# Optimization experiments

Measured on AMD Instinct MI355X. Metric: run time of the kernel, lower is better.

Reference implementation:

```python
import jax, jax.numpy as jnp
import numpy as np
import math

H = 1024
E = 8
K = 2
CF = 1.5
THR = 0.5


def setup_inputs() -> dict:
    key = jax.random.key(0)
    ks = jax.random.split(key, 8)
    s = 0.02
    return {
        'hidden_states': jax.random.normal(ks[0], (2, 2048, H), jnp.float32),
        # importance predictor: Linear(H, H//2) -> ReLU -> Linear(H//2, 1) -> Sigmoid
        'wi1': jax.random.normal(ks[1], (H, H // 2), jnp.float32) * s,
        'bi1': jnp.zeros((H // 2,), jnp.float32),
        'wi2': jax.random.normal(ks[2], (H // 2, 1), jnp.float32) * s,
        'bi2': jnp.zeros((1,), jnp.float32),
        # router_important: Linear(H,H) -> ReLU -> Linear(H,E)
        'wr1': jax.random.normal(ks[3], (H, H), jnp.float32) * s,
        'br1': jnp.zeros((H,), jnp.float32),
        'wr2': jax.random.normal(ks[4], (H, E), jnp.float32) * s,
        'br2': jnp.zeros((E,), jnp.float32),
        # router_unimportant: Linear(H,H) -> ReLU -> Linear(H,E)
        'wu1': jax.random.normal(ks[5], (H, H), jnp.float32) * s,
        'bu1': jnp.zeros((H,), jnp.float32),
        'wu2': jax.random.normal(ks[6], (H, E), jnp.float32) * s,
        'bu2': jnp.zeros((E,), jnp.float32),
    }


def reference(hidden_states, wi1, bi1, wi2, bi2, wr1, br1, wr2, br2, wu1, bu1, wu2, bu2):
    x = hidden_states
    B, S, _ = x.shape
    N = B * S
    capacity = int(B * S * CF * K / E)  # static per-expert capacity

    # dual-gate routing
    importance = jax.nn.sigmoid(jnp.maximum(x @ wi1 + bi1, 0.0) @ wi2 + bi2)  # [B,S,1]
    imp_mask = (importance > THR).astype(x.dtype)                              # [B,S,1]
    logits_imp = jnp.maximum(x @ wr1 + br1, 0.0) @ wr2 + br2                   # [B,S,E]
    logits_unimp = jnp.maximum(x @ wu1 + bu1, 0.0) @ wu2 + bu2                 # [B,S,E]
    router_logits = imp_mask * logits_imp + (1.0 - imp_mask) * logits_unimp
    router_probs = jax.nn.softmax(router_logits, axis=-1)                      # [B,S,E]

    top_k_probs, top_k_indices = jax.lax.top_k(router_probs, K)
    top_k_probs = top_k_probs / top_k_probs.sum(-1, keepdims=True)

    # capacity-constrained dispatch: k-major assignment order (outer loop over k,
    # tokens in order), position within expert = running count, drop if >= capacity
    ef = top_k_indices.reshape(N, K).T.reshape(-1)   # [K*N] expert id, k-major
    pf = top_k_probs.reshape(N, K).T.reshape(-1)     # [K*N] gate prob
    tf = jnp.tile(jnp.arange(N), K)                  # [K*N] token id
    oh = jax.nn.one_hot(ef, E, dtype=jnp.int32)      # [K*N, E]
    pos = jnp.take_along_axis(jnp.cumsum(oh, axis=0), ef[:, None], 1)[:, 0] - 1
    keep = pos < capacity
    posc = jnp.clip(pos, 0, capacity - 1)

    zeros = jnp.zeros((N, E, capacity), x.dtype)
    dispatch = zeros.at[tf, ef, posc].add(keep.astype(x.dtype))
    combine = zeros.at[tf, ef, posc].add(jnp.where(keep, pf, 0.0))
    dispatch = dispatch.reshape(B, S, E, capacity)
    combine = combine.reshape(B, S, E, capacity)

    # aux losses
    rppe = router_probs.mean((0, 1))
    entropy_loss = jnp.sum(rppe * jnp.log(rppe * E + 1e-9))
    imp_sum = (router_probs * imp_mask).sum((0, 1)) + 1e-9
    ippe = imp_sum / imp_sum.sum()
    imp_entropy = -jnp.sum(ippe * jnp.log(ippe + 1e-9))
    aux_loss = entropy_loss - 0.1 * (imp_entropy / math.log(E))

    return dispatch, combine, router_probs, aux_loss, importance
```

## Files before the change

kernel.cpp:

```cpp
#include <hip/hip_runtime.h>
#include <math.h>

#define HDIM  1024
#define HHALF 512
#define NEXP  8
#define NTOK  4096
#define CAP   1536
#define NTOT  2560
#define TOTAL_DC (2u * NTOK * NEXP * CAP)

typedef _Float16 f16x8 __attribute__((ext_vector_type(8)));
typedef float    f32x4 __attribute__((ext_vector_type(4)));

#define GEMM_BLOCKS 640
#define FILL_BLOCKS 1408
#define S_LO 2048.0f
#define S_W  32.0f

__global__ __launch_bounds__(256) void prep(
    const float* __restrict__ x,
    const float* __restrict__ wi1, const float* __restrict__ wr1,
    const float* __restrict__ wu1,
    const float* __restrict__ bi1, const float* __restrict__ br1,
    const float* __restrict__ bu1,
    _Float16* __restrict__ Ah, _Float16* __restrict__ Al,
    _Float16* __restrict__ Bth, _Float16* __restrict__ Btl,
    float* __restrict__ bias_cat)
{
    __shared__ float tile[64][65];
    const int bid = blockIdx.x, tid = threadIdx.x;

    if (bid < 2048) {
        const int i8 = bid * 256 + tid;
        const float4* x4 = (const float4*)x;
        float4 v0 = x4[i8 * 2];
        float4 v1 = x4[i8 * 2 + 1];
        float f[8] = {v0.x, v0.y, v0.z, v0.w, v1.x, v1.y, v1.z, v1.w};
        f16x8 hi, lo;
#pragma unroll
        for (int j = 0; j < 8; j++) {
            _Float16 h = (_Float16)f[j];
            hi[j] = h;
            lo[j] = (_Float16)((f[j] - (float)h) * S_LO);
        }
        *(f16x8*)&Ah[(size_t)i8 * 8] = hi;
        *(f16x8*)&Al[(size_t)i8 * 8] = lo;
        return;
    }
    if (bid < 2688) {
        int local; const float* src; int C, nof;
        int b = bid - 2048;
        if (b < 128)      { src = wi1; C = 512;  nof = 0;    local = b; }
        else if (b < 384) { src = wr1; C = 1024; nof = 512;  local = b - 128; }
        else              { src = wu1; C = 1024; nof = 1536; local = b - 384; }
        const int nti = local >> 4, kti = local & 15;
#pragma unroll
        for (int p = 0; p < 16; p++) {
            int e = p * 256 + tid;
            int kr = e >> 6, nc = e & 63;
            tile[kr][nc] = src[(size_t)(kti * 64 + kr) * C + nti * 64 + nc];
        }
        __syncthreads();
#pragma unroll
        for (int p = 0; p < 16; p++) {
            int e = p * 256 + tid;
            int nl = e >> 6, kk = e & 63;
            float w32 = tile[kk][nl] * S_W;
            _Float16 h = (_Float16)w32;
            _Float16 l = (_Float16)((w32 - (float)h) * S_LO);
            const size_t o = (size_t)(nof + nti * 64 + nl) * 1024 + kti * 64 + kk;
            Bth[o] = h;
            Btl[o] = l;
        }
        return;
    }
    for (int i = tid; i < NTOT; i += 256) {
        float v = (i < 512) ? bi1[i] : (i < 1536) ? br1[i - 512] : bu1[i - 1536];
        bias_cat[i] = v;
    }
}

__global__ __launch_bounds__(256, 2) void gemm_fill(
    const _Float16* __restrict__ Ah, const _Float16* __restrict__ Al,
    const _Float16* __restrict__ Bth, const _Float16* __restrict__ Btl,
    const float* __restrict__ bias_cat,
    const float* __restrict__ wi2, const float* __restrict__ wr2,
    const float* __restrict__ wu2,
    float* __restrict__ part, float* __restrict__ out)
{
    if (blockIdx.x >= GEMM_BLOCKS) {
        f32x4* o4 = (f32x4*)out;
        const unsigned total4 = TOTAL_DC / 4;
        unsigned i = (blockIdx.x - GEMM_BLOCKS) * 256u + threadIdx.x;
        const unsigned stride = FILL_BLOCKS * 256u;
        const f32x4 z = {0.f, 0.f, 0.f, 0.f};
        for (; i < total4; i += stride)
            __builtin_nontemporal_store(z, o4 + i);
        return;
    }

    __shared__ _Float16 lds[2][4][128][32];

    const int tid = threadIdx.x;
    const int lane = tid & 63, wid = tid >> 6;

    const int xcd = blockIdx.x & 7;
    const int idx = blockIdx.x >> 3;
    const int bm  = xcd * 4 + (idx & 3);
    const int bn  = idx >> 2;
    const int rowBase = bm * 128, colBase = bn * 128;

    const _Float16* gb =
        (wid == 0) ? Ah  + (size_t)rowBase * 1024 :
        (wid == 1) ? Al  + (size_t)rowBase * 1024 :
        (wid == 2) ? Bth + (size_t)colBase * 1024 :
                     Btl + (size_t)colBase * 1024;
    const int lrow = lane >> 2;
    const int lkg  = lane & 3;

    f32x4 acc_hh[4][4], acc_x[4][4];
    const f32x4 z4 = {0.f, 0.f, 0.f, 0.f};
#pragma unroll
    for (int i = 0; i < 4; i++)
#pragma unroll
        for (int j = 0; j < 4; j++) { acc_hh[i][j] = z4; acc_x[i][j] = z4; }

    const int mw = (wid >> 1) * 64, nw = (wid & 1) * 64;
    const int fr = lane & 15, s = lane >> 4;

#define STAGE(buf, k0)                                                        \
    {                                                                         \
        _Pragma("unroll")                                                     \
        for (int i = 0; i < 8; i++) {                                         \
            const int r = i * 16 + lrow;                                      \
            __builtin_amdgcn_global_load_lds(                                 \
                (const void*)(gb + (size_t)r * 1024 + (k0) + lkg * 8),        \
                (void*)&lds[buf][wid][i * 16][0], 16, 0, 0);                  \
        }                                                                     \
    }

#define COMPUTE(buf)                                                          \
    {                                                                         \
        f16x8 fa_h[4], fa_l[4], fb_h[4], fb_l[4];                             \
        _Pragma("unroll")                                                     \
        for (int mf = 0; mf < 4; mf++) {                                      \
            fa_h[mf] = *(const f16x8*)&lds[buf][0][mw + mf * 16 + fr][s * 8]; \
            fa_l[mf] = *(const f16x8*)&lds[buf][1][mw + mf * 16 + fr][s * 8]; \
        }                                                                     \
        _Pragma("unroll")                                                     \
        for (int nf = 0; nf < 4; nf++) {                                      \
            fb_h[nf] = *(const f16x8*)&lds[buf][2][nw + nf * 16 + fr][s * 8]; \
            fb_l[nf] = *(const f16x8*)&lds[buf][3][nw + nf * 16 + fr][s * 8]; \
        }                                                                     \
        _Pragma("unroll")                                                     \
        for (int mf = 0; mf < 4; mf++)                                        \
            _Pragma("unroll")                                                 \
            for (int nf = 0; nf < 4; nf++) {                                  \
                acc_hh[mf][nf] = __builtin_amdgcn_mfma_f32_16x16x32_f16(      \
                    fa_h[mf], fb_h[nf], acc_hh[mf][nf], 0, 0, 0);             \
                acc_x[mf][nf] = __builtin_amdgcn_mfma_f32_16x16x32_f16(       \
                    fa_h[mf], fb_l[nf], acc_x[mf][nf], 0, 0, 0);              \
                acc_x[mf][nf] = __builtin_amdgcn_mfma_f32_16x16x32_f16(       \
                    fa_l[mf], fb_h[nf], acc_x[mf][nf], 0, 0, 0);              \
            }                                                                 \
    }

    STAGE(0, 0);
    __syncthreads();

    for (int t = 0; t < 32; t += 2) {
        if (t + 1 < 32) STAGE(1, (t + 1) * 32);
        COMPUTE(0);
        __syncthreads();
        if (t + 2 < 32) STAGE(0, (t + 2) * 32);
        COMPUTE(1);
        __syncthreads();
    }
#undef STAGE
#undef COMPUTE

    const int seg = (bn < 4) ? 0 : (bn < 12 ? 1 : 2);
    const int half = wid & 1;
    float w2v[4][8];
    float bcol[4];
#pragma unroll
    for (int nf = 0; nf < 4; nf++) {
        const int c = colBase + nw + nf * 16 + fr;
        bcol[nf] = bias_cat[c];
        if (seg == 0) {
            w2v[nf][0] = wi2[c];
        } else if (seg == 1) {
            const float4* w4 = (const float4*)&wr2[(c - 512) * 8];
            float4 a = w4[0], b = w4[1];
            w2v[nf][0] = a.x; w2v[nf][1] = a.y; w2v[nf][2] = a.z; w2v[nf][3] = a.w;
            w2v[nf][4] = b.x; w2v[nf][5] = b.y; w2v[nf][6] = b.z; w2v[nf][7] = b.w;
        } else {
            const float4* w4 = (const float4*)&wu2[(c - 1536) * 8];
            float4 a = w4[0], b = w4[1];
            w2v[nf][0] = a.x; w2v[nf][1] = a.y; w2v[nf][2] = a.z; w2v[nf][3] = a.w;
            w2v[nf][4] = b.x; w2v[nf][5] = b.y; w2v[nf][6] = b.z; w2v[nf][7] = b.w;
        }
    }

    const int tgroup = lane >> 4;
#pragma unroll
    for (int mf = 0; mf < 4; mf++) {
        const int tok0 = rowBase + mw + mf * 16 + tgroup * 4;
#pragma unroll
        for (int r = 0; r < 4; r++) {
            float sacc[8];
#pragma unroll
            for (int e = 0; e < 8; e++) sacc[e] = 0.f;
#pragma unroll
            for (int nf = 0; nf < 4; nf++) {
                float v = (acc_hh[mf][nf][r] + acc_x[mf][nf][r] * (1.0f / S_LO))
                          * (1.0f / S_W) + bcol[nf];
                v = fmaxf(v, 0.f);
                if (seg == 0) {
                    sacc[0] = fmaf(v, w2v[nf][0], sacc[0]);
                } else {
#pragma unroll
                    for (int e = 0; e < 8; e++)
                        sacc[e] = fmaf(v, w2v[nf][e], sacc[e]);
                }
            }
            const int nE = (seg == 0) ? 1 : 8;
            for (int e = 0; e < nE; e++) {
                float xv = sacc[e];
                xv += __shfl_xor(xv, 1, 64);
                xv += __shfl_xor(xv, 2, 64);
                xv += __shfl_xor(xv, 4, 64);
                xv += __shfl_xor(xv, 8, 64);
                if (fr == 0)
                    part[(((size_t)bn * 2 + half) * NTOK + (tok0 + r)) * 8 + e] = xv;
            }
        }
    }
}

__global__ __launch_bounds__(256) void reduce_route(
    const float* __restrict__ part,
    const float* __restrict__ bi2, const float* __restrict__ br2,
    const float* __restrict__ bu2,
    float* __restrict__ oprobs, float* __restrict__ oimp,
    int* __restrict__ tke, float* __restrict__ tkp)
{
    const int t = blockIdx.x * 256 + threadIdx.x;

    float imp = bi2[0];
#pragma unroll
    for (int sl = 0; sl < 8; sl++)
        imp += part[((size_t)sl * NTOK + t) * 8];

    float lr[8], lu[8];
#pragma unroll
    for (int e = 0; e < 8; e++) { lr[e] = br2[e]; lu[e] = bu2[e]; }
#pragma unroll
    for (int sl = 8; sl < 24; sl++) {
        const float4* p4 = (const float4*)&part[((size_t)sl * NTOK + t) * 8];
        float4 a = p4[0], b = p4[1];
        lr[0] += a.x; lr[1] += a.y; lr[2] += a.z; lr[3] += a.w;
        lr[4] += b.x; lr[5] += b.y; lr[6] += b.z; lr[7] += b.w;
    }
#pragma unroll
    for (int sl = 24; sl < 40; sl++) {
        const float4* p4 = (const float4*)&part[((size_t)sl * NTOK + t) * 8];
        float4 a = p4[0], b = p4[1];
        lu[0] += a.x; lu[1] += a.y; lu[2] += a.z; lu[3] += a.w;
        lu[4] += b.x; lu[5] += b.y; lu[6] += b.z; lu[7] += b.w;
    }

    const float sig = 1.f / (1.f + expf(-imp));
    oimp[t] = sig;
    const bool m = sig > 0.5f;
    float lg[8];
#pragma unroll
    for (int e = 0; e < 8; e++) lg[e] = m ? lr[e] : lu[e];

    float mx = lg[0];
#pragma unroll
    for (int e = 1; e < 8; e++) mx = fmaxf(mx, lg[e]);
    float p[8], sum = 0.f;
#pragma unroll
    for (int e = 0; e < 8; e++) { p[e] = expf(lg[e] - mx); sum += p[e]; }
    const float inv = 1.f / sum;
#pragma unroll
    for (int e = 0; e < 8; e++) { p[e] *= inv; oprobs[t * 8 + e] = p[e]; }

    int i1 = 0;
#pragma unroll
    for (int e = 1; e < 8; e++) if (p[e] > p[i1]) i1 = e;
    int i2 = (i1 == 0) ? 1 : 0;
#pragma unroll
    for (int e = 0; e < 8; e++) if (e != i1 && p[e] > p[i2]) i2 = e;
    const float ps = p[i1] + p[i2];
    tke[t]        = i1;
    tke[NTOK + t] = i2;
    tkp[t]        = p[i1] / ps;
    tkp[NTOK + t] = p[i2] / ps;
}

__global__ __launch_bounds__(256) void scan_scatter_aux(
    const int* __restrict__ tke, const float* __restrict__ tkp,
    const float* __restrict__ oprobs, const float* __restrict__ oimp,
    float* __restrict__ out, float* __restrict__ oaux)
{
    __shared__ unsigned char se[2 * NTOK];
    __shared__ float         sp[2 * NTOK];
    __shared__ int  cnts[256][8];
    __shared__ float red[4][16];

    const int tid = threadIdx.x;
    const int lane = tid & 63, wv = tid >> 6;

    for (int i = tid; i < 2 * NTOK; i += 256) {
        se[i] = (unsigned char)tke[i];
        sp[i] = tkp[i];
    }

    float ap[8], ai[8];
#pragma unroll
    for (int e = 0; e < 8; e++) { ap[e] = 0.f; ai[e] = 0.f; }
    for (int t = tid; t < NTOK; t += 256) {
        const float msk = (oimp[t] > 0.5f) ? 1.f : 0.f;
#pragma unroll
        for (int e = 0; e < 8; e++) {
            float p = oprobs[t * 8 + e];
            ap[e] += p;
            ai[e] = fmaf(msk, p, ai[e]);
        }
    }
#pragma unroll
    for (int off = 32; off > 0; off >>= 1) {
#pragma unroll
        for (int e = 0; e < 8; e++) {
            ap[e] += __shfl_down(ap[e], off, 64);
            ai[e] += __shfl_down(ai[e], off, 64);
        }
    }
    if (lane == 0) {
#pragma unroll
        for (int e = 0; e < 8; e++) { red[wv][e] = ap[e]; red[wv][8 + e] = ai[e]; }
    }
    __syncthreads();
    if (tid == 0) {
        float ent = 0.f, tot = 0.f, isv[8];
#pragma unroll
        for (int e = 0; e < 8; e++) {
            float spr = red[0][e] + red[1][e] + red[2][e] + red[3][e];
            float sm  = red[0][8 + e] + red[1][8 + e] + red[2][8 + e] + red[3][8 + e];
            float r = spr / (float)NTOK;
            ent += r * logf(r * 8.f + 1e-9f);
            isv[e] = sm + 1e-9f;
            tot += isv[e];
        }
        float ie = 0.f;
#pragma unroll
        for (int e = 0; e < 8; e++) {
            float q = isv[e] / tot;
            ie -= q * logf(q + 1e-9f);
        }
        oaux[0] = ent - 0.1f * (ie / logf(8.f));
    }

    const int base = tid * 32;
    int c[8];
#pragma unroll
    for (int e = 0; e < 8; e++) c[e] = 0;
    for (int i = 0; i < 32; i++) {
        int e = se[base + i];
#pragma unroll
        for (int k = 0; k < 8; k++) c[k] += (e == k) ? 1 : 0;
    }
#pragma unroll
    for (int e = 0; e < 8; e++) cnts[tid][e] = c[e];
    __syncthreads();

    if (tid < 8) {
        int run = 0;
        for (int i = 0; i < 256; i++) {
            int v = cnts[i][tid];
            cnts[i][tid] = run;
            run += v;
        }
    }
    __syncthreads();

    int basecnt[8];
#pragma unroll
    for (int e = 0; e < 8; e++) basecnt[e] = cnts[tid][e];

    float* comb = out + (size_t)NTOK * NEXP * CAP;

    for (int i = 0; i < 32; i++) {
        const int idx = base + i;
        const int e = se[idx];
        int pos = 0;
#pragma unroll
        for (int k = 0; k < 8; k++)
            if (e == k) { pos = basecnt[k]; basecnt[k]++; }
        if (pos < CAP) {
            const int tok = idx & (NTOK - 1);
            const size_t o = ((size_t)tok * NEXP + e) * CAP + pos;
            out[o]  = 1.0f;
            comb[o] = sp[idx];
        }
    }
}

__global__ __launch_bounds__(256) void gemm_bias_relu(
    const float* __restrict__ A, const float* __restrict__ B,
    const float* __restrict__ bias, float* __restrict__ Hout, int N)
{
    __shared__ float As[16][132];
    __shared__ float Bs[16][132];
    const int tid = threadIdx.x;
    const int tx = tid & 15, ty = tid >> 4;
    const int rowBase = blockIdx.y * 128, colBase = blockIdx.x * 128;
    const int lrow = tid >> 1, lkq = (tid & 1) * 8;
    const int bkk = tid >> 4, bcol = (tid & 15) * 8;
    float acc[8][8];
#pragma unroll
    for (int i = 0; i < 8; i++)
#pragma unroll
        for (int j = 0; j < 8; j++) acc[i][j] = 0.f;
    const float* Aptr = A + (size_t)(rowBase + lrow) * HDIM + lkq;
    const float* Bptr = B + (size_t)bkk * N + colBase + bcol;
    for (int k0 = 0; k0 < HDIM; k0 += 16) {
        float4 a0 = *(const float4*)(Aptr + k0);
        float4 a1 = *(const float4*)(Aptr + k0 + 4);
        float4 b0 = *(const float4*)(Bptr + (size_t)k0 * N);
        float4 b1 = *(const float4*)(Bptr + (size_t)k0 * N + 4);
        __syncthreads();
        As[lkq + 0][lrow] = a0.x; As[lkq + 1][lrow] = a0.y;
        As[lkq + 2][lrow] = a0.z; As[lkq + 3][lrow] = a0.w;
        As[lkq + 4][lrow] = a1.x; As[lkq + 5][lrow] = a1.y;
        As[lkq + 6][lrow] = a1.z; As[lkq + 7][lrow] = a1.w;
        *(float4*)&Bs[bkk][bcol] = b0;
        *(float4*)&Bs[bkk][bcol + 4] = b1;
        __syncthreads();
#pragma unroll
        for (int kk = 0; kk < 16; kk++) {
            float4 x0 = *(const float4*)&As[kk][ty * 8];
            float4 x1 = *(const float4*)&As[kk][ty * 8 + 4];
            float4 y0 = *(const float4*)&Bs[kk][tx * 8];
            float4 y1 = *(const float4*)&Bs[kk][tx * 8 + 4];
            float av[8] = {x0.x, x0.y, x0.z, x0.w, x1.x, x1.y, x1.z, x1.w};
            float bv[8] = {y0.x, y0.y, y0.z, y0.w, y1.x, y1.y, y1.z, y1.w};
#pragma unroll
            for (int i = 0; i < 8; i++)
#pragma unroll
                for (int j = 0; j < 8; j++)
                    acc[i][j] = fmaf(av[i], bv[j], acc[i][j]);
        }
    }
#pragma unroll
    for (int i = 0; i < 8; i++) {
        const int r = rowBase + ty * 8 + i, c = colBase + tx * 8;
#pragma unroll
        for (int j = 0; j < 8; j += 4) {
            float4 v;
            v.x = fmaxf(acc[i][j + 0] + bias[c + j + 0], 0.f);
            v.y = fmaxf(acc[i][j + 1] + bias[c + j + 1], 0.f);
            v.z = fmaxf(acc[i][j + 2] + bias[c + j + 2], 0.f);
            v.w = fmaxf(acc[i][j + 3] + bias[c + j + 3], 0.f);
            *(float4*)&Hout[(size_t)r * N + c + j] = v;
        }
    }
}

__global__ __launch_bounds__(256) void zerofill_fb(float* __restrict__ out)
{
    f32x4* o4 = (f32x4*)out;
    const unsigned total4 = TOTAL_DC / 4;
    unsigned i = blockIdx.x * 256u + threadIdx.x;
    const unsigned stride = gridDim.x * 256u;
    const f32x4 z = {0.f, 0.f, 0.f, 0.f};
    for (; i < total4; i += stride) o4[i] = z;
}

__global__ __launch_bounds__(256) void second_layer_sep(
    const float* __restrict__ h_i, const float* __restrict__ h_r,
    const float* __restrict__ h_u,
    const float* __restrict__ wi2, const float* __restrict__ bi2,
    const float* __restrict__ wr2, const float* __restrict__ br2,
    const float* __restrict__ wu2, const float* __restrict__ bu2,
    float* __restrict__ oprobs, float* __restrict__ oimp,
    int* __restrict__ tke, float* __restrict__ tkp)
{
    const int t = blockIdx.x;
    const int tid = threadIdx.x;
    float pi = 0.f;
    float pr[8], pu[8];
#pragma unroll
    for (int e = 0; e < 8; e++) { pr[e] = 0.f; pu[e] = 0.f; }
    const float* hi = h_i + (size_t)t * HHALF;
    const float* hr = h_r + (size_t)t * HDIM;
    const float* hu = h_u + (size_t)t * HDIM;
    for (int j = tid; j < HHALF; j += 256) pi = fmaf(hi[j], wi2[j], pi);
    for (int j = tid; j < HDIM; j += 256) {
        float a = hr[j], b = hu[j];
#pragma unroll
        for (int e = 0; e < 8; e++) {
            pr[e] = fmaf(a, wr2[j * 8 + e], pr[e]);
            pu[e] = fmaf(b, wu2[j * 8 + e], pu[e]);
        }
    }
#pragma unroll
    for (int off = 32; off > 0; off >>= 1) {
        pi += __shfl_down(pi, off, 64);
#pragma unroll
        for (int e = 0; e < 8; e++) {
            pr[e] += __shfl_down(pr[e], off, 64);
            pu[e] += __shfl_down(pu[e], off, 64);
        }
    }
    __shared__ float red[4][17];
    const int lane = tid & 63, wv = tid >> 6;
    if (lane == 0) {
        red[wv][0] = pi;
#pragma unroll
        for (int e = 0; e < 8; e++) { red[wv][1 + e] = pr[e]; red[wv][9 + e] = pu[e]; }
    }
    __syncthreads();
    if (tid == 0) {
        float si = red[0][0] + red[1][0] + red[2][0] + red[3][0] + bi2[0];
        float sig = 1.f / (1.f + expf(-si));
        oimp[t] = sig;
        const bool m = sig > 0.5f;
        float lg[8];
#pragma unroll
        for (int e = 0; e < 8; e++) {
            float vr = red[0][1 + e] + red[1][1 + e] + red[2][1 + e] + red[3][1 + e] + br2[e];
            float vu = red[0][9 + e] + red[1][9 + e] + red[2][9 + e] + red[3][9 + e] + bu2[e];
            lg[e] = m ? vr : vu;
        }
        float mx = lg[0];
#pragma unroll
        for (int e = 1; e < 8; e++) mx = fmaxf(mx, lg[e]);
        float p[8], s = 0.f;
#pragma unroll
        for (int e = 0; e < 8; e++) { p[e] = expf(lg[e] - mx); s += p[e]; }
        const float inv = 1.f / s;
#pragma unroll
        for (int e = 0; e < 8; e++) { p[e] *= inv; oprobs[t * 8 + e] = p[e]; }
        int i1 = 0;
#pragma unroll
        for (int e = 1; e < 8; e++) if (p[e] > p[i1]) i1 = e;
        int i2 = (i1 == 0) ? 1 : 0;
#pragma unroll
        for (int e = 0; e < 8; e++) if (e != i1 && p[e] > p[i2]) i2 = e;
        const float ps = p[i1] + p[i2];
        tke[t]        = i1;
        tke[NTOK + t] = i2;
        tkp[t]        = p[i1] / ps;
        tkp[NTOK + t] = p[i2] / ps;
    }
}

extern "C" void kernel_launch(void* const* d_in, const int* in_sizes, int n_in,
                              void* d_out, int out_size, void* d_ws, size_t ws_size,
                              hipStream_t stream) {
    const float* x   = (const float*)d_in[0];
    const float* wi1 = (const float*)d_in[1];
    const float* bi1 = (const float*)d_in[2];
    const float* wi2 = (const float*)d_in[3];
    const float* bi2 = (const float*)d_in[4];
    const float* wr1 = (const float*)d_in[5];
    const float* br1 = (const float*)d_in[6];
    const float* wr2 = (const float*)d_in[7];
    const float* br2 = (const float*)d_in[8];
    const float* wu1 = (const float*)d_in[9];
    const float* bu1 = (const float*)d_in[10];
    const float* wu2 = (const float*)d_in[11];
    const float* bu2 = (const float*)d_in[12];

    float* out    = (float*)d_out;
    float* oprobs = out + (size_t)TOTAL_DC;
    float* oaux   = oprobs + NTOK * NEXP;
    float* oimp   = oaux + 1;

    const size_t szA  = (size_t)NTOK * HDIM * 2;
    const size_t szB  = (size_t)NTOT * HDIM * 2;
    const size_t szP  = (size_t)40 * NTOK * 8 * 4;
    const size_t need = 2 * szA + 2 * szB + NTOT * 4 + szP
                      + 2 * NTOK * 4 + 2 * NTOK * 4 + 4096;
    dim3 blk(256);

    if (ws_size >= need) {
        char* p = (char*)d_ws;
        _Float16* Ah   = (_Float16*)p;         p += szA;
        _Float16* Al   = (_Float16*)p;         p += szA;
        _Float16* Bth  = (_Float16*)p;         p += szB;
        _Float16* Btl  = (_Float16*)p;         p += szB;
        float*    bias = (float*)p;            p += NTOT * 4;
        float*    part = (float*)p;            p += szP;
        int*      tke  = (int*)p;              p += 2 * NTOK * 4;
        float*    tkp  = (float*)p;

        prep<<<2689, blk, 0, stream>>>(x, wi1, wr1, wu1, bi1, br1, bu1,
                                       Ah, Al, Bth, Btl, bias);
        gemm_fill<<<GEMM_BLOCKS + FILL_BLOCKS, blk, 0, stream>>>(
            Ah, Al, Bth, Btl, bias, wi2, wr2, wu2, part, out);
        reduce_route<<<NTOK / 256, blk, 0, stream>>>(
            part, bi2, br2, bu2, oprobs, oimp, tke, tkp);
        scan_scatter_aux<<<1, blk, 0, stream>>>(tke, tkp, oprobs, oimp, out, oaux);
    } else {
        float* h_i = out;
        float* h_r = h_i + (size_t)NTOK * HHALF;
        float* h_u = h_r + (size_t)NTOK * HDIM;
        int*   tke  = (int*)d_ws;
        float* tkp  = (float*)d_ws + 2 * NTOK;

        gemm_bias_relu<<<dim3(HHALF / 128, NTOK / 128), blk, 0, stream>>>(x, wi1, bi1, h_i, HHALF);
        gemm_bias_relu<<<dim3(HDIM / 128, NTOK / 128), blk, 0, stream>>>(x, wr1, br1, h_r, HDIM);
        gemm_bias_relu<<<dim3(HDIM / 128, NTOK / 128), blk, 0, stream>>>(x, wu1, bu1, h_u, HDIM);
        second_layer_sep<<<NTOK, blk, 0, stream>>>(h_i, h_r, h_u, wi2, bi2, wr2, br2,
                                                   wu2, bu2, oprobs, oimp, tke, tkp);
        zerofill_fb<<<2048, blk, 0, stream>>>(out);
        scan_scatter_aux<<<1, blk, 0, stream>>>(tke, tkp, oprobs, oimp, out, oaux);
    }
}
```

Measured before the change: 186.1 us.

## Interleave GEMM and zero-fill blocks and XOR-swizzle LDS tile layout

```diff
diff --git a/kernel.cpp b/kernel.cpp
--- a/kernel.cpp
+++ b/kernel.cpp
@@ -12,7 +12,6 @@
 typedef _Float16 f16x8 __attribute__((ext_vector_type(8)));
 typedef float    f32x4 __attribute__((ext_vector_type(4)));
 
-#define GEMM_BLOCKS 640
 #define FILL_BLOCKS 1408
 #define S_LO 2048.0f
 #define S_W  32.0f
@@ -88,10 +87,17 @@
     const float* __restrict__ wu2,
     float* __restrict__ part, float* __restrict__ out)
 {
-    if (blockIdx.x >= GEMM_BLOCKS) {
+    const int o = blockIdx.x >> 3, sub = blockIdx.x & 7;
+    const int k = o >> 3, j = o & 7;
+    int g = -1, fo = 0;
+    if (k < 11)       { if (j < 7) g = k * 7 + j; else fo = k; }
+    else if (k == 11) { if (j < 3) g = 77 + j;    else fo = 11 + (j - 3); }
+    else              { fo = 16 + ((k - 12) << 3) + j; }
+
+    if (g < 0) {
         f32x4* o4 = (f32x4*)out;
         const unsigned total4 = TOTAL_DC / 4;
-        unsigned i = (blockIdx.x - GEMM_BLOCKS) * 256u + threadIdx.x;
+        unsigned i = (unsigned)(fo * 8 + sub) * 256u + threadIdx.x;
         const unsigned stride = FILL_BLOCKS * 256u;
         const f32x4 z = {0.f, 0.f, 0.f, 0.f};
         for (; i < total4; i += stride)
@@ -104,10 +110,8 @@
     const int tid = threadIdx.x;
     const int lane = tid & 63, wid = tid >> 6;
 
-    const int xcd = blockIdx.x & 7;
-    const int idx = blockIdx.x >> 3;
-    const int bm  = xcd * 4 + (idx & 3);
-    const int bn  = idx >> 2;
+    const int bm  = sub * 4 + (g & 3);
+    const int bn  = g >> 2;
     const int rowBase = bm * 128, colBase = bn * 128;
 
     const _Float16* gb =
@@ -116,17 +120,18 @@
         (wid == 2) ? Bth + (size_t)colBase * 1024 :
                      Btl + (size_t)colBase * 1024;
     const int lrow = lane >> 2;
-    const int lkg  = lane & 3;
+    const int lkgs = (lane & 3) ^ ((lane >> 3) & 3);
 
     f32x4 acc_hh[4][4], acc_x[4][4];
     const f32x4 z4 = {0.f, 0.f, 0.f, 0.f};
 #pragma unroll
     for (int i = 0; i < 4; i++)
 #pragma unroll
-        for (int j = 0; j < 4; j++) { acc_hh[i][j] = z4; acc_x[i][j] = z4; }
+        for (int j2 = 0; j2 < 4; j2++) { acc_hh[i][j2] = z4; acc_x[i][j2] = z4; }
 
     const int mw = (wid >> 1) * 64, nw = (wid & 1) * 64;
     const int fr = lane & 15, s = lane >> 4;
+    const int rs = s ^ ((fr >> 1) & 3);
 
 #define STAGE(buf, k0)                                                        \
     {                                                                         \
@@ -134,7 +139,7 @@
         for (int i = 0; i < 8; i++) {                                         \
             const int r = i * 16 + lrow;                                      \
             __builtin_amdgcn_global_load_lds(                                 \
-                (const void*)(gb + (size_t)r * 1024 + (k0) + lkg * 8),        \
+                (const void*)(gb + (size_t)r * 1024 + (k0) + lkgs * 8),       \
                 (void*)&lds[buf][wid][i * 16][0], 16, 0, 0);                  \
         }                                                                     \
     }
@@ -144,13 +149,13 @@
         f16x8 fa_h[4], fa_l[4], fb_h[4], fb_l[4];                             \
         _Pragma("unroll")                                                     \
         for (int mf = 0; mf < 4; mf++) {                                      \
-            fa_h[mf] = *(const f16x8*)&lds[buf][0][mw + mf * 16 + fr][s * 8]; \
-            fa_l[mf] = *(const f16x8*)&lds[buf][1][mw + mf * 16 + fr][s * 8]; \
+            fa_h[mf] = *(const f16x8*)&lds[buf][0][mw + mf * 16 + fr][rs * 8];\
+            fa_l[mf] = *(const f16x8*)&lds[buf][1][mw + mf * 16 + fr][rs * 8];\
         }                                                                     \
         _Pragma("unroll")                                                     \
         for (int nf = 0; nf < 4; nf++) {                                      \
-            fb_h[nf] = *(const f16x8*)&lds[buf][2][nw + nf * 16 + fr][s * 8]; \
-            fb_l[nf] = *(const f16x8*)&lds[buf][3][nw + nf * 16 + fr][s * 8]; \
+            fb_h[nf] = *(const f16x8*)&lds[buf][2][nw + nf * 16 + fr][rs * 8];\
+            fb_l[nf] = *(const f16x8*)&lds[buf][3][nw + nf * 16 + fr][rs * 8];\
         }                                                                     \
         _Pragma("unroll")                                                     \
         for (int mf = 0; mf < 4; mf++)                                        \
@@ -600,7 +605,7 @@
 
         prep<<<2689, blk, 0, stream>>>(x, wi1, wr1, wu1, bi1, br1, bu1,
                                        Ah, Al, Bth, Btl, bias);
-        gemm_fill<<<GEMM_BLOCKS + FILL_BLOCKS, blk, 0, stream>>>(
+        gemm_fill<<<2048, blk, 0, stream>>>(
             Ah, Al, Bth, Btl, bias, wi2, wr2, wu2, part, out);
         reduce_route<<<NTOK / 256, blk, 0, stream>>>(
             part, bi2, br2, bu2, oprobs, oimp, tke, tkp);
```

After: 212.1 us. 1.14x slower.
